# Performance work log

Hardware: AMD Instinct MI355X
Metric: run time of the kernel (lower is better)

Reference implementation:

```python
import jax, jax.numpy as jnp
import numpy as np

N = 262144
IN_DIM = 1024
HID = 256
E = 16
TOP_K = 2


def setup_inputs() -> dict:
    key = jax.random.key(0)
    k1, k2, k3, k4, k5 = jax.random.split(key, 5)
    x = jax.random.normal(k1, (N, IN_DIM), dtype=jnp.float32)
    # Kaiming-ish init scaled for stability
    W1 = jax.random.normal(k2, (IN_DIM, HID), dtype=jnp.float32) * (1.0 / np.sqrt(IN_DIM))
    b1 = jnp.zeros((HID,), dtype=jnp.float32)
    W2 = jax.random.normal(k3, (HID, E), dtype=jnp.float32) * (1.0 / np.sqrt(HID))
    b2 = jnp.zeros((E,), dtype=jnp.float32)
    return {"x": x, "W1": W1, "b1": b1, "W2": W2, "b2": b2}


def reference(x, W1, b1, W2, b2):
    # MLP router: Linear -> ELU -> Linear
    h = jax.nn.elu(x @ W1 + b1)            # [N, HID]
    logits = h @ W2 + b2                   # [N, E]
    # top-k mask: keep top-k logits, set the rest to -inf (scatter semantics)
    vals, idx = jax.lax.top_k(logits, TOP_K)          # [N, K]
    rows = jnp.arange(logits.shape[0])[:, None]        # [N, 1]
    masked = jnp.full_like(logits, -jnp.inf).at[rows, idx].set(vals)
    alpha = jax.nn.softmax(masked, axis=-1)            # [N, E]
    return alpha, logits
```

## Files before the change

kernel.cpp:

```cpp
#include <hip/hip_runtime.h>
#include <math.h>

#define KDIM 1024
#define HID 256
#define NE 16
#define NROWS_BLK 128
#define KCH 64
#define NCHUNK (KDIM / KCH)
#define W1T_PLANE (HID * KDIM)
#define W2T_PLANE (NE * HID)
#define SMEM_BYTES 131072

typedef __attribute__((ext_vector_type(8))) _Float16 f16x8;
typedef __attribute__((ext_vector_type(16))) float f32x16;
typedef __attribute__((ext_vector_type(4))) float f32x4;

__global__ void prep_w1(const float* __restrict__ W1, _Float16* __restrict__ w1t) {
  int idx = blockIdx.x * 256 + threadIdx.x;
  int col = idx >> 7, k8 = (idx & 127) * 8;
  f16x8 p1, p2;
#pragma unroll
  for (int i = 0; i < 8; ++i) {
    float v = W1[(size_t)(k8 + i) * HID + col];
    _Float16 a = (_Float16)v;
    _Float16 b = (_Float16)((v - (float)a) * 4096.0f);
    p1[i] = a; p2[i] = b;
  }
  size_t off = (size_t)col * KDIM + k8;
  *(f16x8*)(w1t + off) = p1;
  *(f16x8*)(w1t + W1T_PLANE + off) = p2;
}

__global__ void prep_w2(const float* __restrict__ W2, _Float16* __restrict__ w2t) {
  int idx = blockIdx.x * 256 + threadIdx.x;
  int e = idx & 15, k = idx >> 4;
  float v = W2[(size_t)k * NE + e];
  _Float16 a = (_Float16)v;
  _Float16 b = (_Float16)((v - (float)a) * 4096.0f);
  w2t[(size_t)e * HID + k] = a;
  w2t[W2T_PLANE + (size_t)e * HID + k] = b;
}


__global__ __launch_bounds__(512, 2) void fused_router(
    const float* __restrict__ x, const _Float16* __restrict__ w1t,
    const _Float16* __restrict__ w2t, const float* __restrict__ b1,
    const float* __restrict__ b2, float* __restrict__ outA,
    float* __restrict__ outL)
{
  extern __shared__ char smem[];
  const int t = threadIdx.x;
  const int l = t & 63;
  const int w = t >> 6;
  const int rowg = w >> 2, colg = w & 3;
  const int l31 = l & 31, hi = l >> 5;
  const int R0 = blockIdx.x * NROWS_BLK;

  const int arow0 = rowg * 64 + l31;
  const int bcol0 = colg * 64 + l31;
  const int s7 = l31 & 7;

  const int xr = t >> 2, xg0 = (t & 3) * 2, xs7 = xr & 7;
  const float* xbase = x + (size_t)(R0 + xr) * KDIM + (t & 3) * 16;

  const int bp = t >> 8, bcol = t & 255, bc7 = bcol & 7;
  const _Float16* bsrc0 = w1t + (size_t)bp * W1T_PLANE + (size_t)bcol * KDIM;

  f32x16 acc0[2][2], accA[2][2];
#pragma unroll
  for (int rt = 0; rt < 2; ++rt)
#pragma unroll
    for (int ct = 0; ct < 2; ++ct) {
#pragma unroll
      for (int j = 0; j < 16; ++j) { acc0[rt][ct][j] = 0.f; accA[rt][ct][j] = 0.f; }
    }

  float xvA[16], xvB[16];

#define XLOAD(XV_, TC_) do {                                                  \
    _Pragma("unroll") for (int i_ = 0; i_ < 4; ++i_)                          \
      *(float4*)((XV_) + 4 * i_) =                                            \
        *(const float4*)(xbase + (size_t)(TC_) * KCH + 4 * i_);               \
  } while (0)

#define STAGE(TC_, XV_) do {                                                  \
    const int abw_ = ((TC_) & 1) * 32768;                                     \
    const _Float16* ws_ = bsrc0 + (size_t)(TC_) * KCH;                        \
    f16x8 bst_[8];                                                            \
    _Pragma("unroll") for (int i_ = 0; i_ < 8; ++i_)                          \
      bst_[i_] = *(const f16x8*)(ws_ + 8 * i_);                               \
    f16x8 a1lo_, a1hi_, a2lo_, a2hi_;                                         \
    _Pragma("unroll") for (int j_ = 0; j_ < 16; ++j_) {                       \
      float v_ = (XV_)[j_];                                                   \
      _Float16 h1_ = (_Float16)v_;                                            \
      _Float16 h2_ = (_Float16)((v_ - (float)h1_) * 4096.0f);                 \
      if (j_ < 8) { a1lo_[j_ & 7] = h1_; a2lo_[j_ & 7] = h2_; }               \
      else        { a1hi_[j_ & 7] = h1_; a2hi_[j_ & 7] = h2_; }               \
    }                                                                         \
    *(f16x8*)(smem + abw_ + xr * 128 + ((xg0 ^ xs7) << 4)) = a1lo_;           \
    *(f16x8*)(smem + abw_ + xr * 128 + (((xg0 + 1) ^ xs7) << 4)) = a1hi_;     \
    *(f16x8*)(smem + abw_ + 16384 + xr * 128 + ((xg0 ^ xs7) << 4)) = a2lo_;   \
    *(f16x8*)(smem + abw_ + 16384 + xr * 128 + (((xg0 + 1) ^ xs7) << 4)) = a2hi_; \
    _Pragma("unroll") for (int i_ = 0; i_ < 8; ++i_)                          \
      *(f16x8*)(smem + 65536 + bp * 32768 + bcol * 128 + ((i_ ^ bc7) << 4)) = bst_[i_]; \
  } while (0)

#define COMPUTE(TC_, PREF_, XV_) do {                                         \
    const int abr_ = ((TC_) & 1) * 32768;                                     \
    if (PREF_) { XLOAD(XV_, (TC_) + 2); }                                     \
    _Pragma("unroll") for (int s_ = 0; s_ < 4; ++s_) {                        \
      const int gg_ = (2 * s_ + hi) ^ s7;                                     \
      f16x8 a1f_[2], a2f_[2], b1f_[2], b2f_[2];                               \
      _Pragma("unroll") for (int rt_ = 0; rt_ < 2; ++rt_) {                   \
        int ro_ = (arow0 + rt_ * 32) * 128 + (gg_ << 4);                      \
        a1f_[rt_] = *(const f16x8*)(smem + abr_ + ro_);                       \
        a2f_[rt_] = *(const f16x8*)(smem + abr_ + 16384 + ro_);               \
      }                                                                       \
      _Pragma("unroll") for (int ct_ = 0; ct_ < 2; ++ct_) {                   \
        int co_ = (bcol0 + ct_ * 32) * 128 + (gg_ << 4);                      \
        b1f_[ct_] = *(const f16x8*)(smem + 65536 + co_);                      \
        b2f_[ct_] = *(const f16x8*)(smem + 98304 + co_);                      \
      }                                                                       \
      _Pragma("unroll") for (int rt_ = 0; rt_ < 2; ++rt_)                     \
      _Pragma("unroll") for (int ct_ = 0; ct_ < 2; ++ct_) {                   \
        acc0[rt_][ct_] = __builtin_amdgcn_mfma_f32_32x32x16_f16(              \
            a1f_[rt_], b1f_[ct_], acc0[rt_][ct_], 0, 0, 0);                   \
        accA[rt_][ct_] = __builtin_amdgcn_mfma_f32_32x32x16_f16(              \
            a1f_[rt_], b2f_[ct_], accA[rt_][ct_], 0, 0, 0);                   \
        accA[rt_][ct_] = __builtin_amdgcn_mfma_f32_32x32x16_f16(              \
            a2f_[rt_], b1f_[ct_], accA[rt_][ct_], 0, 0, 0);                   \
      }                                                                       \
    }                                                                         \
  } while (0)

  XLOAD(xvA, 0);
  XLOAD(xvB, 1);
  STAGE(0, xvA);
  __syncthreads();

#pragma unroll 1
  for (int tcb = 0; tcb < NCHUNK; tcb += 2) {
    COMPUTE(tcb, tcb + 2 < NCHUNK, xvA);
    __syncthreads();
    STAGE(tcb + 1, xvB);
    __syncthreads();
    COMPUTE(tcb + 1, tcb + 3 < NCHUNK, xvB);
    __syncthreads();
    if (tcb + 2 < NCHUNK) STAGE(tcb + 2, xvA);
    __syncthreads();
  }

  const float c12 = 1.0f / 4096.0f;
#pragma unroll
  for (int ct = 0; ct < 2; ++ct) {
    int col = bcol0 + ct * 32;
    float bc = b1[col];
    int cg = col >> 3, cb = (col & 7) * 2;
#pragma unroll
    for (int rt = 0; rt < 2; ++rt) {
#pragma unroll
      for (int r = 0; r < 16; ++r) {
        int row = rowg * 64 + rt * 32 + (r & 3) + 8 * (r >> 2) + 4 * hi;
        float v = acc0[rt][ct][r] + c12 * accA[rt][ct][r] + bc;
        v = v > 0.f ? v : expm1f(v);
        _Float16 h1 = (_Float16)v;
        _Float16 h2 = (_Float16)((v - (float)h1) * 4096.0f);
        int off = row * 512 + ((cg ^ (row & 7)) << 4) + cb;
        *(_Float16*)(smem + off) = h1;
        *(_Float16*)(smem + 65536 + off) = h2;
      }
    }
  }
  __syncthreads();

  const int tok = l & 15, g2 = l >> 4;
  const int hrow = w * 16 + tok;
  f32x4 L0, LA;
#pragma unroll
  for (int j = 0; j < 4; ++j) { L0[j] = 0.f; LA[j] = 0.f; }
  const _Float16* w2a = w2t + (size_t)(l & 15) * HID;
  const _Float16* w2b = w2a + W2T_PLANE;
#pragma unroll
  for (int kt = 0; kt < 8; ++kt) {
    int gg = (kt * 4 + g2) ^ (hrow & 7);
    f16x8 hb1 = *(const f16x8*)(smem + hrow * 512 + (gg << 4));
    f16x8 hb2 = *(const f16x8*)(smem + 65536 + hrow * 512 + (gg << 4));
    f16x8 wa = *(const f16x8*)(w2a + kt * 32 + 8 * g2);
    f16x8 wb = *(const f16x8*)(w2b + kt * 32 + 8 * g2);
    L0 = __builtin_amdgcn_mfma_f32_16x16x32_f16(wa, hb1, L0, 0, 0, 0);
    LA = __builtin_amdgcn_mfma_f32_16x16x32_f16(wa, hb2, LA, 0, 0, 0);
    LA = __builtin_amdgcn_mfma_f32_16x16x32_f16(wb, hb1, LA, 0, 0, 0);
  }

  float4 b2v = *(const float4*)(b2 + 4 * g2);
  float L[4];
  L[0] = L0[0] + c12 * LA[0] + b2v.x;
  L[1] = L0[1] + c12 * LA[1] + b2v.y;
  L[2] = L0[2] + c12 * LA[2] + b2v.z;
  L[3] = L0[3] + c12 * LA[3] + b2v.w;

  float o1[4], o2[4], o3[4];
#pragma unroll
  for (int j = 0; j < 4; ++j) o1[j] = __shfl_xor(L[j], 16);
#pragma unroll
  for (int j = 0; j < 4; ++j) o2[j] = __shfl_xor(L[j], 32);
#pragma unroll
  for (int j = 0; j < 4; ++j) o3[j] = __shfl_xor(o1[j], 32);

  float all16[16];
#pragma unroll
  for (int c = 0; c < 4; ++c) {
    int xg = c ^ g2;
#pragma unroll
    for (int j = 0; j < 4; ++j) {
      float v = L[j];
      v = (xg == 1) ? o1[j] : v;
      v = (xg == 2) ? o2[j] : v;
      v = (xg == 3) ? o3[j] : v;
      all16[c * 4 + j] = v;
    }
  }

  int i1 = 0; float m1 = all16[0];
#pragma unroll
  for (int e = 1; e < 16; ++e) { if (all16[e] > m1) { m1 = all16[e]; i1 = e; } }
  int i2 = -1; float m2 = -INFINITY;
#pragma unroll
  for (int e = 0; e < 16; ++e) { if (e != i1 && all16[e] > m2) { m2 = all16[e]; i2 = e; } }
  float ex = expf(m2 - m1);
  float sden = 1.f + ex;
  float A1 = 1.f / sden;
  float A2 = ex / sden;

  int e0 = 4 * g2;
  float4 alv;
  alv.x = (e0 + 0 == i1) ? A1 : ((e0 + 0 == i2) ? A2 : 0.f);
  alv.y = (e0 + 1 == i1) ? A1 : ((e0 + 1 == i2) ? A2 : 0.f);
  alv.z = (e0 + 2 == i1) ? A1 : ((e0 + 2 == i2) ? A2 : 0.f);
  alv.w = (e0 + 3 == i1) ? A1 : ((e0 + 3 == i2) ? A2 : 0.f);

  size_t orow = (size_t)(R0 + w * 16 + tok);
  float4 lgv; lgv.x = L[0]; lgv.y = L[1]; lgv.z = L[2]; lgv.w = L[3];
  *(float4*)(outL + orow * NE + e0) = lgv;
  *(float4*)(outA + orow * NE + e0) = alv;
}

extern "C" void kernel_launch(void* const* d_in, const int* in_sizes, int n_in,
                              void* d_out, int out_size, void* d_ws, size_t ws_size,
                              hipStream_t stream) {
  const float* x  = (const float*)d_in[0];
  const float* W1 = (const float*)d_in[1];
  const float* b1 = (const float*)d_in[2];
  const float* W2 = (const float*)d_in[3];
  const float* b2 = (const float*)d_in[4];
  _Float16* w1t = (_Float16*)d_ws;
  _Float16* w2t = w1t + 2 * W1T_PLANE;
  float* outA = (float*)d_out;
  const size_t n_tok = (size_t)in_sizes[0] / KDIM;
  float* outL = outA + n_tok * NE;

  prep_w1<<<dim3(128), dim3(256), 0, stream>>>(W1, w1t);
  prep_w2<<<dim3(16), dim3(256), 0, stream>>>(W2, w2t);

  hipFuncSetAttribute((const void*)fused_router,
                      hipFuncAttributeMaxDynamicSharedMemorySize, SMEM_BYTES);
  fused_router<<<dim3((unsigned)(n_tok / NROWS_BLK)), dim3(512), SMEM_BYTES, stream>>>(
      x, w1t, w2t, b1, b2, outA, outL);
}
```

Before: 675.6 us.

## Stream pre-tiled W1 chunks to LDS via global_load_lds with single-sync double buffering

Pre-arranges the split-fp16 W1 into per-chunk images laid out exactly as LDS expects, so each block copies them with asynchronous global_load_lds instead of loading through registers. The block tile shrinks to 64 rows and the K chunk to 32, with double-buffered LDS and one barrier per iteration rather than four. Launch bounds now request 4 blocks per CU for more occupancy. In exchange, each block re-reads W1 for half as many rows, which doubles W1 traffic from L2. The tighter register budget also risks spills.

```diff
diff --git a/kernel.cpp b/kernel.cpp
--- a/kernel.cpp
+++ b/kernel.cpp
@@ -4,20 +4,30 @@
 #define KDIM 1024
 #define HID 256
 #define NE 16
-#define NROWS_BLK 128
-#define KCH 64
-#define NCHUNK (KDIM / KCH)
-#define W1T_PLANE (HID * KDIM)
+#define ROWS_BLK 64
+#define KCH 32
+#define NCHUNK 32
+#define CH_BYTES 32768
 #define W2T_PLANE (NE * HID)
-#define SMEM_BYTES 131072
-
+#define BBASE 16384
+#define BB_STRIDE 32768
+#define SMEM_BYTES 81920
+
+typedef __attribute__((ext_vector_type(4))) _Float16 f16x4;
 typedef __attribute__((ext_vector_type(8))) _Float16 f16x8;
 typedef __attribute__((ext_vector_type(16))) float f32x16;
 typedef __attribute__((ext_vector_type(4))) float f32x4;
 
-__global__ void prep_w1(const float* __restrict__ W1, _Float16* __restrict__ w1t) {
+__device__ __forceinline__ void gld16(const void* g, void* s) {
+  __builtin_amdgcn_global_load_lds(
+      (const __attribute__((address_space(1))) void*)g,
+      (__attribute__((address_space(3))) void*)s, 16, 0, 0);
+}
+
+__global__ void prep_w1(const float* __restrict__ W1, _Float16* __restrict__ img) {
   int idx = blockIdx.x * 256 + threadIdx.x;
-  int col = idx >> 7, k8 = (idx & 127) * 8;
+  int col = idx & 255, kgl = idx >> 8;
+  int c = kgl >> 2, kg = kgl & 3, k8 = kgl * 8;
   f16x8 p1, p2;
 #pragma unroll
   for (int i = 0; i < 8; ++i) {
@@ -26,9 +36,9 @@
     _Float16 b = (_Float16)((v - (float)a) * 4096.0f);
     p1[i] = a; p2[i] = b;
   }
-  size_t off = (size_t)col * KDIM + k8;
-  *(f16x8*)(w1t + off) = p1;
-  *(f16x8*)(w1t + W1T_PLANE + off) = p2;
+  size_t off = (size_t)c * 16384 + (size_t)kg * 2048 + (size_t)col * 8;
+  *(f16x8*)(img + off) = p1;
+  *(f16x8*)(img + off + 8192) = p2;
 }
 
 __global__ void prep_w2(const float* __restrict__ W2, _Float16* __restrict__ w2t) {
@@ -41,208 +51,195 @@
   w2t[W2T_PLANE + (size_t)e * HID + k] = b;
 }
 
-
-__global__ __launch_bounds__(512, 2) void fused_router(
-    const float* __restrict__ x, const _Float16* __restrict__ w1t,
-    const _Float16* __restrict__ w2t, const float* __restrict__ b1,
-    const float* __restrict__ b2, float* __restrict__ outA,
+__global__ __launch_bounds__(512, 4) void fused_router(
+    const float* __restrict__ x, const _Float16* __restrict__ w1img,
+    const _Float16* __restrict__ w2t, const float* __restrict__ bias1,
+    const float* __restrict__ bias2, float* __restrict__ outA,
     float* __restrict__ outL)
 {
   extern __shared__ char smem[];
-  const int t = threadIdx.x;
-  const int l = t & 63;
-  const int w = t >> 6;
+  const int t = threadIdx.x, l = t & 63, w = t >> 6;
   const int rowg = w >> 2, colg = w & 3;
   const int l31 = l & 31, hi = l >> 5;
-  const int R0 = blockIdx.x * NROWS_BLK;
-
-  const int arow0 = rowg * 64 + l31;
+  const int R0 = blockIdx.x * ROWS_BLK;
+  const int arow = rowg * 32 + l31;
   const int bcol0 = colg * 64 + l31;
-  const int s7 = l31 & 7;
-
-  const int xr = t >> 2, xg0 = (t & 3) * 2, xs7 = xr & 7;
-  const float* xbase = x + (size_t)(R0 + xr) * KDIM + (t & 3) * 16;
-
-  const int bp = t >> 8, bcol = t & 255, bc7 = bcol & 7;
-  const _Float16* bsrc0 = w1t + (size_t)bp * W1T_PLANE + (size_t)bcol * KDIM;
-
-  f32x16 acc0[2][2], accA[2][2];
-#pragma unroll
-  for (int rt = 0; rt < 2; ++rt)
-#pragma unroll
-    for (int ct = 0; ct < 2; ++ct) {
-#pragma unroll
-      for (int j = 0; j < 16; ++j) { acc0[rt][ct][j] = 0.f; accA[rt][ct][j] = 0.f; }
-    }
-
-  float xvA[16], xvB[16];
-
-#define XLOAD(XV_, TC_) do {                                                  \
-    _Pragma("unroll") for (int i_ = 0; i_ < 4; ++i_)                          \
-      *(float4*)((XV_) + 4 * i_) =                                            \
-        *(const float4*)(xbase + (size_t)(TC_) * KCH + 4 * i_);               \
+
+  const int xr = t >> 3, xq = t & 7;
+  const float* xbase = x + (size_t)(R0 + xr) * KDIM + xq * 4;
+  const int akg = xq >> 1, asub = (xq & 1) * 8;
+
+  const char* ibase = (const char*)w1img + t * 16;
+
+  f32x16 acc0[2], accA[2];
+#pragma unroll
+  for (int ct = 0; ct < 2; ++ct)
+#pragma unroll
+    for (int j = 0; j < 16; ++j) { acc0[ct][j] = 0.f; accA[ct][j] = 0.f; }
+
+  float4 xv;
+
+#define XLOAD(C_) do { xv = *(const float4*)(xbase + (size_t)(C_) * KCH); } while (0)
+
+#define BSTAGE(C_, BS_) do {                                                  \
+    const char* is_ = ibase + (size_t)(C_) * CH_BYTES;                        \
+    char* bd_ = smem + BBASE + (BS_) * BB_STRIDE + t * 16;                    \
+    gld16(is_,         bd_);                                                  \
+    gld16(is_ + 8192,  bd_ + 8192);                                           \
+    gld16(is_ + 16384, bd_ + 16384);                                          \
+    gld16(is_ + 24576, bd_ + 24576);                                          \
   } while (0)
 
-#define STAGE(TC_, XV_) do {                                                  \
-    const int abw_ = ((TC_) & 1) * 32768;                                     \
-    const _Float16* ws_ = bsrc0 + (size_t)(TC_) * KCH;                        \
-    f16x8 bst_[8];                                                            \
-    _Pragma("unroll") for (int i_ = 0; i_ < 8; ++i_)                          \
-      bst_[i_] = *(const f16x8*)(ws_ + 8 * i_);                               \
-    f16x8 a1lo_, a1hi_, a2lo_, a2hi_;                                         \
-    _Pragma("unroll") for (int j_ = 0; j_ < 16; ++j_) {                       \
-      float v_ = (XV_)[j_];                                                   \
-      _Float16 h1_ = (_Float16)v_;                                            \
-      _Float16 h2_ = (_Float16)((v_ - (float)h1_) * 4096.0f);                 \
-      if (j_ < 8) { a1lo_[j_ & 7] = h1_; a2lo_[j_ & 7] = h2_; }               \
-      else        { a1hi_[j_ & 7] = h1_; a2hi_[j_ & 7] = h2_; }               \
+#define ASPLIT(BS_) do {                                                      \
+    float vals_[4] = {xv.x, xv.y, xv.z, xv.w};                                \
+    f16x4 pa_, pb_;                                                           \
+    _Pragma("unroll") for (int j_ = 0; j_ < 4; ++j_) {                        \
+      float v_ = vals_[j_];                                                   \
+      _Float16 a_ = (_Float16)v_;                                             \
+      _Float16 b_ = (_Float16)((v_ - (float)a_) * 4096.0f);                   \
+      pa_[j_] = a_; pb_[j_] = b_;                                             \
     }                                                                         \
-    *(f16x8*)(smem + abw_ + xr * 128 + ((xg0 ^ xs7) << 4)) = a1lo_;           \
-    *(f16x8*)(smem + abw_ + xr * 128 + (((xg0 + 1) ^ xs7) << 4)) = a1hi_;     \
-    *(f16x8*)(smem + abw_ + 16384 + xr * 128 + ((xg0 ^ xs7) << 4)) = a2lo_;   \
-    *(f16x8*)(smem + abw_ + 16384 + xr * 128 + (((xg0 + 1) ^ xs7) << 4)) = a2hi_; \
-    _Pragma("unroll") for (int i_ = 0; i_ < 8; ++i_)                          \
-      *(f16x8*)(smem + 65536 + bp * 32768 + bcol * 128 + ((i_ ^ bc7) << 4)) = bst_[i_]; \
+    int ao_ = (BS_) * 8192 + akg * 1024 + xr * 16 + asub;                     \
+    *(f16x4*)(smem + ao_) = pa_;                                              \
+    *(f16x4*)(smem + ao_ + 4096) = pb_;                                       \
   } while (0)
 
-#define COMPUTE(TC_, PREF_, XV_) do {                                         \
-    const int abr_ = ((TC_) & 1) * 32768;                                     \
-    if (PREF_) { XLOAD(XV_, (TC_) + 2); }                                     \
-    _Pragma("unroll") for (int s_ = 0; s_ < 4; ++s_) {                        \
-      const int gg_ = (2 * s_ + hi) ^ s7;                                     \
-      f16x8 a1f_[2], a2f_[2], b1f_[2], b2f_[2];                               \
-      _Pragma("unroll") for (int rt_ = 0; rt_ < 2; ++rt_) {                   \
-        int ro_ = (arow0 + rt_ * 32) * 128 + (gg_ << 4);                      \
-        a1f_[rt_] = *(const f16x8*)(smem + abr_ + ro_);                       \
-        a2f_[rt_] = *(const f16x8*)(smem + abr_ + 16384 + ro_);               \
-      }                                                                       \
+#define COMPUTE(BS_) do {                                                     \
+    _Pragma("unroll") for (int s_ = 0; s_ < 2; ++s_) {                        \
+      const int gg_ = 2 * s_ + hi;                                            \
+      int ao_ = (BS_) * 8192 + gg_ * 1024 + arow * 16;                        \
+      f16x8 a1_ = *(const f16x8*)(smem + ao_);                                \
+      f16x8 a2_ = *(const f16x8*)(smem + ao_ + 4096);                         \
       _Pragma("unroll") for (int ct_ = 0; ct_ < 2; ++ct_) {                   \
-        int co_ = (bcol0 + ct_ * 32) * 128 + (gg_ << 4);                      \
-        b1f_[ct_] = *(const f16x8*)(smem + 65536 + co_);                      \
-        b2f_[ct_] = *(const f16x8*)(smem + 98304 + co_);                      \
-      }                                                                       \
-      _Pragma("unroll") for (int rt_ = 0; rt_ < 2; ++rt_)                     \
-      _Pragma("unroll") for (int ct_ = 0; ct_ < 2; ++ct_) {                   \
-        acc0[rt_][ct_] = __builtin_amdgcn_mfma_f32_32x32x16_f16(              \
-            a1f_[rt_], b1f_[ct_], acc0[rt_][ct_], 0, 0, 0);                   \
-        accA[rt_][ct_] = __builtin_amdgcn_mfma_f32_32x32x16_f16(              \
-            a1f_[rt_], b2f_[ct_], accA[rt_][ct_], 0, 0, 0);                   \
-        accA[rt_][ct_] = __builtin_amdgcn_mfma_f32_32x32x16_f16(              \
-            a2f_[rt_], b1f_[ct_], accA[rt_][ct_], 0, 0, 0);                   \
+        int bo_ = BBASE + (BS_) * BB_STRIDE + gg_ * 4096                      \
+                  + (bcol0 + 32 * ct_) * 16;                                  \
+        f16x8 b1_ = *(const f16x8*)(smem + bo_);                              \
+        f16x8 b2_ = *(const f16x8*)(smem + bo_ + 16384);                      \
+        acc0[ct_] = __builtin_amdgcn_mfma_f32_32x32x16_f16(                   \
+            a1_, b1_, acc0[ct_], 0, 0, 0);                                    \
+        accA[ct_] = __builtin_amdgcn_mfma_f32_32x32x16_f16(                   \
+            a1_, b2_, accA[ct_], 0, 0, 0);                                    \
+        accA[ct_] = __builtin_amdgcn_mfma_f32_32x32x16_f16(                   \
+            a2_, b1_, accA[ct_], 0, 0, 0);                                    \
       }                                                                       \
     }                                                                         \
   } while (0)
 
-  XLOAD(xvA, 0);
-  XLOAD(xvB, 1);
-  STAGE(0, xvA);
+  XLOAD(0);
+  BSTAGE(0, 0);
+  ASPLIT(0);
+  XLOAD(1);
   __syncthreads();
 
+  int bsel = 0;
 #pragma unroll 1
-  for (int tcb = 0; tcb < NCHUNK; tcb += 2) {
-    COMPUTE(tcb, tcb + 2 < NCHUNK, xvA);
+  for (int c = 0; c < NCHUNK; ++c) {
+    if (c + 1 < NCHUNK) {
+      BSTAGE(c + 1, bsel ^ 1);
+      ASPLIT(bsel ^ 1);
+      if (c + 2 < NCHUNK) XLOAD(c + 2);
+    }
+    COMPUTE(bsel);
     __syncthreads();
-    STAGE(tcb + 1, xvB);
-    __syncthreads();
-    COMPUTE(tcb + 1, tcb + 3 < NCHUNK, xvB);
-    __syncthreads();
-    if (tcb + 2 < NCHUNK) STAGE(tcb + 2, xvA);
-    __syncthreads();
+    bsel ^= 1;
   }
 
   const float c12 = 1.0f / 4096.0f;
+  const int tok = l & 15, g2 = l >> 4;
+
 #pragma unroll
   for (int ct = 0; ct < 2; ++ct) {
-    int col = bcol0 + ct * 32;
-    float bc = b1[col];
+    int col = bcol0 + 32 * ct;
+    float bc = bias1[col];
     int cg = col >> 3, cb = (col & 7) * 2;
 #pragma unroll
-    for (int rt = 0; rt < 2; ++rt) {
-#pragma unroll
-      for (int r = 0; r < 16; ++r) {
-        int row = rowg * 64 + rt * 32 + (r & 3) + 8 * (r >> 2) + 4 * hi;
-        float v = acc0[rt][ct][r] + c12 * accA[rt][ct][r] + bc;
-        v = v > 0.f ? v : expm1f(v);
-        _Float16 h1 = (_Float16)v;
-        _Float16 h2 = (_Float16)((v - (float)h1) * 4096.0f);
-        int off = row * 512 + ((cg ^ (row & 7)) << 4) + cb;
-        *(_Float16*)(smem + off) = h1;
-        *(_Float16*)(smem + 65536 + off) = h2;
+    for (int r = 0; r < 16; ++r) {
+      int row = rowg * 32 + (r & 3) + 8 * (r >> 2) + 4 * hi;
+      float v = acc0[ct][r] + c12 * accA[ct][r] + bc;
+      v = v > 0.f ? v : expm1f(v);
+      _Float16 h1 = (_Float16)v;
+      _Float16 h2 = (_Float16)((v - (float)h1) * 4096.0f);
+      int off = row * 512 + ((cg ^ (row & 7)) << 4) + cb;
+      *(_Float16*)(smem + off) = h1;
+      *(_Float16*)(smem + 32768 + off) = h2;
+    }
+  }
+  __syncthreads();
+
+  if (w < 4) {
+    int tloc = w * 16 + tok;
+    f32x4 L0, LA;
+#pragma unroll
+    for (int j = 0; j < 4; ++j) { L0[j] = 0.f; LA[j] = 0.f; }
+    const _Float16* w2a = w2t + (size_t)tok * HID;
+    const _Float16* w2b = w2a + W2T_PLANE;
+#pragma unroll
+    for (int kt = 0; kt < 8; ++kt) {
+      int gg = (kt * 4 + g2) ^ (tloc & 7);
+      f16x8 hb1 = *(const f16x8*)(smem + tloc * 512 + (gg << 4));
+      f16x8 hb2 = *(const f16x8*)(smem + 32768 + tloc * 512 + (gg << 4));
+      f16x8 wa = *(const f16x8*)(w2a + kt * 32 + 8 * g2);
+      f16x8 wb = *(const f16x8*)(w2b + kt * 32 + 8 * g2);
+      L0 = __builtin_amdgcn_mfma_f32_16x16x32_f16(wa, hb1, L0, 0, 0, 0);
+      LA = __builtin_amdgcn_mfma_f32_16x16x32_f16(wa, hb2, LA, 0, 0, 0);
+      LA = __builtin_amdgcn_mfma_f32_16x16x32_f16(wb, hb1, LA, 0, 0, 0);
+    }
+    float4 b2v = *(const float4*)(bias2 + 4 * g2);
+    float L[4];
+    L[0] = L0[0] + c12 * LA[0] + b2v.x;
+    L[1] = L0[1] + c12 * LA[1] + b2v.y;
+    L[2] = L0[2] + c12 * LA[2] + b2v.z;
+    L[3] = L0[3] + c12 * LA[3] + b2v.w;
+
+    float o1[4], o2[4], o3[4];
+#pragma unroll
+    for (int j = 0; j < 4; ++j) o1[j] = __shfl_xor(L[j], 16);
+#pragma unroll
+    for (int j = 0; j < 4; ++j) o2[j] = __shfl_xor(L[j], 32);
+#pragma unroll
+    for (int j = 0; j < 4; ++j) o3[j] = __shfl_xor(o1[j], 32);
+
+    float all16[16];
+#pragma unroll
+    for (int cq = 0; cq < 4; ++cq) {
+      int xg = cq ^ g2;
+#pragma unroll
+      for (int j = 0; j < 4; ++j) {
+        float v = L[j];
+        v = (xg == 1) ? o1[j] : v;
+        v = (xg == 2) ? o2[j] : v;
+        v = (xg == 3) ? o3[j] : v;
+        all16[cq * 4 + j] = v;
       }
     }
-  }
-  __syncthreads();
-
-  const int tok = l & 15, g2 = l >> 4;
-  const int hrow = w * 16 + tok;
-  f32x4 L0, LA;
-#pragma unroll
-  for (int j = 0; j < 4; ++j) { L0[j] = 0.f; LA[j] = 0.f; }
-  const _Float16* w2a = w2t + (size_t)(l & 15) * HID;
-  const _Float16* w2b = w2a + W2T_PLANE;
-#pragma unroll
-  for (int kt = 0; kt < 8; ++kt) {
-    int gg = (kt * 4 + g2) ^ (hrow & 7);
-    f16x8 hb1 = *(const f16x8*)(smem + hrow * 512 + (gg << 4));
-    f16x8 hb2 = *(const f16x8*)(smem + 65536 + hrow * 512 + (gg << 4));
-    f16x8 wa = *(const f16x8*)(w2a + kt * 32 + 8 * g2);
-    f16x8 wb = *(const f16x8*)(w2b + kt * 32 + 8 * g2);
-    L0 = __builtin_amdgcn_mfma_f32_16x16x32_f16(wa, hb1, L0, 0, 0, 0);
-    LA = __builtin_amdgcn_mfma_f32_16x16x32_f16(wa, hb2, LA, 0, 0, 0);
-    LA = __builtin_amdgcn_mfma_f32_16x16x32_f16(wb, hb1, LA, 0, 0, 0);
-  }
-
-  float4 b2v = *(const float4*)(b2 + 4 * g2);
-  float L[4];
-  L[0] = L0[0] + c12 * LA[0] + b2v.x;
-  L[1] = L0[1] + c12 * LA[1] + b2v.y;
-  L[2] = L0[2] + c12 * LA[2] + b2v.z;
-  L[3] = L0[3] + c12 * LA[3] + b2v.w;
-
-  float o1[4], o2[4], o3[4];
-#pragma unroll
-  for (int j = 0; j < 4; ++j) o1[j] = __shfl_xor(L[j], 16);
-#pragma unroll
-  for (int j = 0; j < 4; ++j) o2[j] = __shfl_xor(L[j], 32);
-#pragma unroll
-  for (int j = 0; j < 4; ++j) o3[j] = __shfl_xor(o1[j], 32);
-
-  float all16[16];
-#pragma unroll
-  for (int c = 0; c < 4; ++c) {
-    int xg = c ^ g2;
-#pragma unroll
-    for (int j = 0; j < 4; ++j) {
-      float v = L[j];
-      v = (xg == 1) ? o1[j] : v;
-      v = (xg == 2) ? o2[j] : v;
-      v = (xg == 3) ? o3[j] : v;
-      all16[c * 4 + j] = v;
-    }
-  }
-
-  int i1 = 0; float m1 = all16[0];
-#pragma unroll
-  for (int e = 1; e < 16; ++e) { if (all16[e] > m1) { m1 = all16[e]; i1 = e; } }
-  int i2 = -1; float m2 = -INFINITY;
-#pragma unroll
-  for (int e = 0; e < 16; ++e) { if (e != i1 && all16[e] > m2) { m2 = all16[e]; i2 = e; } }
-  float ex = expf(m2 - m1);
-  float sden = 1.f + ex;
-  float A1 = 1.f / sden;
-  float A2 = ex / sden;
-
-  int e0 = 4 * g2;
-  float4 alv;
-  alv.x = (e0 + 0 == i1) ? A1 : ((e0 + 0 == i2) ? A2 : 0.f);
-  alv.y = (e0 + 1 == i1) ? A1 : ((e0 + 1 == i2) ? A2 : 0.f);
-  alv.z = (e0 + 2 == i1) ? A1 : ((e0 + 2 == i2) ? A2 : 0.f);
-  alv.w = (e0 + 3 == i1) ? A1 : ((e0 + 3 == i2) ? A2 : 0.f);
-
-  size_t orow = (size_t)(R0 + w * 16 + tok);
-  float4 lgv; lgv.x = L[0]; lgv.y = L[1]; lgv.z = L[2]; lgv.w = L[3];
-  *(float4*)(outL + orow * NE + e0) = lgv;
-  *(float4*)(outA + orow * NE + e0) = alv;
+
+    int i1 = 0; float m1 = all16[0];
+#pragma unroll
+    for (int e = 1; e < 16; ++e) { if (all16[e] > m1) { m1 = all16[e]; i1 = e; } }
+    int i2 = -1; float m2 = -INFINITY;
+#pragma unroll
+    for (int e = 0; e < 16; ++e) { if (e != i1 && all16[e] > m2) { m2 = all16[e]; i2 = e; } }
+    float ex = expf(m2 - m1);
+    float sden = 1.f + ex;
+    float A1 = 1.f / sden;
+    float A2 = ex / sden;
+
+    int e0 = 4 * g2;
+    float4 alv;
+    alv.x = (e0 + 0 == i1) ? A1 : ((e0 + 0 == i2) ? A2 : 0.f);
+    alv.y = (e0 + 1 == i1) ? A1 : ((e0 + 1 == i2) ? A2 : 0.f);
+    alv.z = (e0 + 2 == i1) ? A1 : ((e0 + 2 == i2) ? A2 : 0.f);
+    alv.w = (e0 + 3 == i1) ? A1 : ((e0 + 3 == i2) ? A2 : 0.f);
+
+    size_t orow = (size_t)(R0 + tloc);
+    float4 lgv; lgv.x = L[0]; lgv.y = L[1]; lgv.z = L[2]; lgv.w = L[3];
+    *(float4*)(outL + orow * NE + e0) = lgv;
+    *(float4*)(outA + orow * NE + e0) = alv;
+  }
+#undef XLOAD
+#undef BSTAGE
+#undef ASPLIT
+#undef COMPUTE
 }
 
 extern "C" void kernel_launch(void* const* d_in, const int* in_sizes, int n_in,
@@ -253,17 +250,17 @@
   const float* b1 = (const float*)d_in[2];
   const float* W2 = (const float*)d_in[3];
   const float* b2 = (const float*)d_in[4];
-  _Float16* w1t = (_Float16*)d_ws;
-  _Float16* w2t = w1t + 2 * W1T_PLANE;
+  _Float16* w1img = (_Float16*)d_ws;
+  _Float16* w2t = w1img + (size_t)NCHUNK * (CH_BYTES / 2);
   float* outA = (float*)d_out;
   const size_t n_tok = (size_t)in_sizes[0] / KDIM;
   float* outL = outA + n_tok * NE;
 
-  prep_w1<<<dim3(128), dim3(256), 0, stream>>>(W1, w1t);
+  prep_w1<<<dim3(128), dim3(256), 0, stream>>>(W1, w1img);
   prep_w2<<<dim3(16), dim3(256), 0, stream>>>(W2, w2t);
 
   hipFuncSetAttribute((const void*)fused_router,
                       hipFuncAttributeMaxDynamicSharedMemorySize, SMEM_BYTES);
-  fused_router<<<dim3((unsigned)(n_tok / NROWS_BLK)), dim3(512), SMEM_BYTES, stream>>>(
-      x, w1t, w2t, b1, b2, outA, outL);
-}
+  fused_router<<<dim3((unsigned)(n_tok / ROWS_BLK)), dim3(512), SMEM_BYTES, stream>>>(
+      x, w1img, w2t, b1, b2, outA, outL);
+}
```

New measurement: 575.6 us. -14.8%, faster.
